# Kernel tuning notes

Hardware: AMD Instinct MI355X
Metric: run time of the kernel (lower is better)

The kernel has to match this reference:

```python
import jax, jax.numpy as jnp
import numpy as np
from jax import lax


def _conv(x, w, padding):
    # NCHW conv, stride 1
    return lax.conv_general_dilated(
        x, w, window_strides=(1, 1), padding=padding,
        dimension_numbers=("NCHW", "OIHW", "NCHW"))


def setup_inputs() -> dict:
    key = jax.random.key(0)
    ks = jax.random.split(key, 6)
    B, C_IN, H, W = 128, 2, 64, 64
    L_H, L_Q = 150, 10
    return {
        "X":   jax.random.normal(ks[0], (B, C_IN, H, W), jnp.float32),
        "h_w": jax.random.normal(ks[1], (L_H, C_IN, 3, 3), jnp.float32) * 0.1,
        "h_b": jax.random.normal(ks[2], (L_H,), jnp.float32) * 0.1,
        "r_w": jax.random.normal(ks[3], (1, L_H, 1, 1), jnp.float32) * 0.1,
        "q_w": jax.random.normal(ks[4], (L_Q, 1, 3, 3), jnp.float32) * 0.1,
        "w":   jax.random.normal(ks[5], (L_Q, 1, 3, 3), jnp.float32) * 0.1,
        "k":   40,
    }


def reference(X, h_w, h_b, r_w, q_w, w, k):
    # h = Conv3x3(X) + bias ; r = Conv1x1(h) ; q = Conv3x3(r)
    h = _conv(X, h_w, "SAME") + h_b[None, :, None, None]   # [B, l_h, H, W]
    r = _conv(h, r_w, "VALID")                             # [B, 1, H, W]
    q = _conv(r, q_w, "SAME")                              # [B, l_q, H, W]
    v = jnp.max(q, axis=1, keepdims=True)                  # [B, 1, H, W]

    qw_cat = jnp.concatenate([q_w, w], axis=1)             # [l_q, 2, 3, 3]

    def body(i, v):
        rv = jnp.concatenate([r, v], axis=1)               # [B, 2, H, W]
        q = _conv(rv, qw_cat, "SAME")                      # [B, l_q, H, W]
        return jnp.max(q, axis=1, keepdims=True)

    v = lax.fori_loop(0, k - 1, body, v)
    return v
```

## Files before the change

### kernel.cpp

```cpp
#include <hip/hip_runtime.h>

typedef float f2 __attribute__((ext_vector_type(2)));

#define HW 64
#define XR (66*64)
#define LH 150
#define LQ 10

__device__ __forceinline__ float dpp_wshr1(float x) {
    return __builtin_bit_cast(float, __builtin_amdgcn_update_dpp(
        0, __builtin_bit_cast(int, x), 0x138, 0xF, 0xF, true));
}
__device__ __forceinline__ float dpp_wshl1(float x) {
    return __builtin_bit_cast(float, __builtin_amdgcn_update_dpp(
        0, __builtin_bit_cast(int, x), 0x130, 0xF, 0xF, true));
}
__device__ __forceinline__ f2 dpp2_shr(f2 v) { return (f2){dpp_wshr1(v.x), dpp_wshr1(v.y)}; }
__device__ __forceinline__ f2 dpp2_shl(f2 v) { return (f2){dpp_wshl1(v.x), dpp_wshl1(v.y)}; }

__device__ __forceinline__ f2 pk_fma_b0(f2 a, f2 wpair, f2 c) {
    f2 d;
    asm("v_pk_fma_f32 %0, %1, %2, %3 op_sel_hi:[1,0,1]"
        : "=v"(d) : "v"(a), "s"(wpair), "v"(c));
    return d;
}
__device__ __forceinline__ f2 pk_fma_b1(f2 a, f2 wpair, f2 c) {
    f2 d;
    asm("v_pk_fma_f32 %0, %1, %2, %3 op_sel:[0,1,0]"
        : "=v"(d) : "v"(a), "s"(wpair), "v"(c));
    return d;
}

__global__ __launch_bounds__(1024)
void vin_main(const float* __restrict__ X,
              const float* __restrict__ h_w,
              const float* __restrict__ h_b,
              const float* __restrict__ r_w,
              const float* __restrict__ q_w,
              const float* __restrict__ wgt,
              const int* __restrict__ kptr,
              float* __restrict__ out) {
    __shared__ float smem[3*XR + 32];
    float* sR  = smem + 2*XR;
    float* sWE = smem + 3*XR;
    float* sHB = smem;
    float* sHT = smem + 2176;

    const int b = blockIdx.x, tid = threadIdx.x;
    const int w = tid >> 6, l = tid & 63;

    for (int i = tid; i < 3*XR + 32; i += 1024) smem[i] = 0.f;
    __syncthreads();

    #pragma unroll
    for (int i = 0; i < 2; ++i) {
        int j = w + 16*i;
        if (j < 19) {
            float s = 0.f;
            #pragma unroll
            for (int u = 0; u < 3; ++u) {
                int t = l + 64*u;
                if (t < LH) {
                    float src = (j < 18) ? h_w[t*18 + j] : h_b[t];
                    s = fmaf(r_w[t], src, s);
                }
            }
            #pragma unroll
            for (int off = 32; off >= 1; off >>= 1)
                s += __shfl_xor(s, off);
            if (l == 0) sWE[j] = s;
        }
    }

    const float* Xb = X + (size_t)b * 2 * HW * HW;
    for (int i = tid; i < 2*64*16; i += 1024) {
        int ch = i >> 10, j = i & 1023, row = j >> 4, c = j & 15;
        float4 v = *(const float4*)(Xb + ((size_t)ch*HW + row)*HW + c*4);
        *(float4*)(smem + ch*XR + (row+1)*64 + c*4) = v;
    }
    __syncthreads();

    float wE[19];
    #pragma unroll
    for (int i = 0; i < 19; ++i) wE[i] = sWE[i];
    float rloc[4];
    {
        float xc[2][6], xl[2][6], xr[2][6];
        #pragma unroll
        for (int ch = 0; ch < 2; ++ch)
            #pragma unroll
            for (int k = 0; k < 6; ++k) {
                xc[ch][k] = smem[ch*XR + (4*w + k)*64 + l];
                xl[ch][k] = dpp_wshr1(xc[ch][k]);
                xr[ch][k] = dpp_wshl1(xc[ch][k]);
            }
        #pragma unroll
        for (int i = 0; i < 4; ++i) {
            float acc = wE[18];
            #pragma unroll
            for (int ch = 0; ch < 2; ++ch)
                #pragma unroll
                for (int dy = 0; dy < 3; ++dy) {
                    acc = fmaf(xl[ch][i+dy], wE[ch*9 + dy*3 + 0], acc);
                    acc = fmaf(xc[ch][i+dy], wE[ch*9 + dy*3 + 1], acc);
                    acc = fmaf(xr[ch][i+dy], wE[ch*9 + dy*3 + 2], acc);
                }
            rloc[i] = acc;
        }
    }
    #pragma unroll
    for (int i = 0; i < 4; ++i) sR[(4*w + i + 1)*64 + l] = rloc[i];
    __syncthreads();

    f2 qr[LQ][2];
    f2 vc[2];
    {
        float rc[6], rl[6], rr2[6];
        #pragma unroll
        for (int k = 0; k < 6; ++k) {
            rc[k]  = sR[(4*w + k)*64 + l];
            rl[k]  = dpp_wshr1(rc[k]);
            rr2[k] = dpp_wshl1(rc[k]);
        }
        float vcur[4];
        #pragma unroll
        for (int a = 0; a < LQ; ++a) {
            float qa[9];
            #pragma unroll
            for (int i = 0; i < 9; ++i) qa[i] = q_w[a*9 + i];
            float acc[4];
            #pragma unroll
            for (int i = 0; i < 4; ++i) {
                float s = 0.f;
                #pragma unroll
                for (int dy = 0; dy < 3; ++dy) {
                    s = fmaf(rl[i+dy],  qa[dy*3 + 0], s);
                    s = fmaf(rc[i+dy],  qa[dy*3 + 1], s);
                    s = fmaf(rr2[i+dy], qa[dy*3 + 2], s);
                }
                acc[i] = s;
                vcur[i] = a ? fmaxf(vcur[i], s) : s;
            }
            qr[a][0] = (f2){acc[0], acc[1]};
            qr[a][1] = (f2){acc[2], acc[3]};
        }
        vc[0] = (f2){vcur[0], vcur[1]};
        vc[1] = (f2){vcur[2], vcur[3]};
    }
    if (tid < 256) {
        int p = tid >> 7, half = (tid >> 6) & 1, ll = tid & 63;
        if (half == 0) sHB[p*1088 + 0*64  + ll] = 0.f;
        else           sHT[p*1088 + 16*64 + ll] = 0.f;
    }

    f2 wv2[LQ][5];
    #pragma unroll
    for (int a = 0; a < LQ; ++a) {
        #pragma unroll
        for (int p = 0; p < 4; ++p)
            wv2[a][p] = (f2){wgt[a*9 + 2*p], wgt[a*9 + 2*p + 1]};
        wv2[a][4] = (f2){wgt[a*9 + 8], 0.f};
    }

    const int km1 = kptr[0] - 1;
    const int wrB = (w+1)*64 + l;
    const int wrT = w*64 + l;
    for (int t = 0; t < km1; ++t) {
        const int p = (t & 1) * 1088;
        sHB[p + wrB] = vc[1].y;
        sHT[p + wrT] = vc[0].x;
        __syncthreads();
        float ht = sHB[p + wrT];
        float hb = sHT[p + wrB];

        f2 P[3];
        P[0] = (f2){ht,       vc[0].x};
        P[1] = (f2){vc[0].y,  vc[1].x};
        P[2] = (f2){vc[1].y,  hb};
        f2 PL[3], PR[3], OL[2], OR[2];
        #pragma unroll
        for (int j = 0; j < 3; ++j) { PL[j] = dpp2_shr(P[j]); PR[j] = dpp2_shl(P[j]); }
        #pragma unroll
        for (int j = 0; j < 2; ++j) { OL[j] = dpp2_shr(vc[j]); OR[j] = dpp2_shl(vc[j]); }

        f2 vn[2];
        #pragma unroll
        for (int a = 0; a < LQ; ++a) {
            #pragma unroll
            for (int j = 0; j < 2; ++j) {
                f2 acc = qr[a][j];
                acc = pk_fma_b0(PL[j],   wv2[a][0], acc);
                acc = pk_fma_b1(P[j],    wv2[a][0], acc);
                acc = pk_fma_b0(PR[j],   wv2[a][1], acc);
                acc = pk_fma_b1(OL[j],   wv2[a][1], acc);
                acc = pk_fma_b0(vc[j],   wv2[a][2], acc);
                acc = pk_fma_b1(OR[j],   wv2[a][2], acc);
                acc = pk_fma_b0(PL[j+1], wv2[a][3], acc);
                acc = pk_fma_b1(P[j+1],  wv2[a][3], acc);
                acc = pk_fma_b0(PR[j+1], wv2[a][4], acc);
                vn[j] = (a == 0) ? acc : __builtin_elementwise_max(vn[j], acc);
            }
        }
        vc[0] = vn[0]; vc[1] = vn[1];
    }

    float* ob = out + (size_t)b*HW*HW + (size_t)(4*w)*HW + l;
    ob[0*HW] = vc[0].x;
    ob[1*HW] = vc[0].y;
    ob[2*HW] = vc[1].x;
    ob[3*HW] = vc[1].y;
}

extern "C" void kernel_launch(void* const* d_in, const int* in_sizes, int n_in,
                              void* d_out, int out_size, void* d_ws, size_t ws_size,
                              hipStream_t stream) {
    const float* X   = (const float*)d_in[0];
    const float* h_w = (const float*)d_in[1];
    const float* h_b = (const float*)d_in[2];
    const float* r_w = (const float*)d_in[3];
    const float* q_w = (const float*)d_in[4];
    const float* w   = (const float*)d_in[5];
    const int*   k   = (const int*)d_in[6];
    float* out = (float*)d_out;

    vin_main<<<128, 1024, 0, stream>>>(X, h_w, h_b, r_w, q_w, w, k, out);
}
```

Baseline: 146.3 us.

## Split each image across two blocks with global-memory halo exchange

Each image is now split into top and bottom halves, one per block, so the launch grows from 128 to 256 blocks and fills more compute units. Each thread now handles 2 rows instead of 4. At every iteration the boundary rows are exchanged between the paired blocks through a global buffer of tagged 64-bit atomics, with spin-waits on the iteration tag. This doubles parallelism at the cost of a per-iteration cross-block global round trip and a memset launch, and it relies on both blocks of a pair being co-resident to avoid deadlock.

After: 123.4 us. 15.7% less time.

```diff
diff --git a/kernel.cpp b/kernel.cpp
--- a/kernel.cpp
+++ b/kernel.cpp
@@ -3,9 +3,14 @@
 typedef float f2 __attribute__((ext_vector_type(2)));
 
 #define HW 64
-#define XR (66*64)
 #define LH 150
 #define LQ 10
+
+#define X36R (36*64)
+#define R34  (34*64)
+#define SMEM_TOT (2*X36R + R34 + 32)
+
+__device__ unsigned long long g_halo[2*2*128*64];
 
 __device__ __forceinline__ float dpp_wshr1(float x) {
     return __builtin_bit_cast(float, __builtin_amdgcn_update_dpp(
@@ -40,16 +45,19 @@
               const float* __restrict__ wgt,
               const int* __restrict__ kptr,
               float* __restrict__ out) {
-    __shared__ float smem[3*XR + 32];
-    float* sR  = smem + 2*XR;
-    float* sWE = smem + 3*XR;
+    __shared__ float smem[SMEM_TOT];
+    float* sR  = smem + 2*X36R;
+    float* sWE = smem + 2*X36R + R34;
     float* sHB = smem;
     float* sHT = smem + 2176;
 
-    const int b = blockIdx.x, tid = threadIdx.x;
+    const int bid = blockIdx.x;
+    const int img = bid & 127, half = bid >> 7;
+    const int base = half << 5;
+    const int tid = threadIdx.x;
     const int w = tid >> 6, l = tid & 63;
 
-    for (int i = tid; i < 3*XR + 32; i += 1024) smem[i] = 0.f;
+    for (int i = tid; i < SMEM_TOT; i += 1024) smem[i] = 0.f;
     __syncthreads();
 
     #pragma unroll
@@ -72,65 +80,59 @@
         }
     }
 
-    const float* Xb = X + (size_t)b * 2 * HW * HW;
-    for (int i = tid; i < 2*64*16; i += 1024) {
-        int ch = i >> 10, j = i & 1023, row = j >> 4, c = j & 15;
-        float4 v = *(const float4*)(Xb + ((size_t)ch*HW + row)*HW + c*4);
-        *(float4*)(smem + ch*XR + (row+1)*64 + c*4) = v;
+    const float* Xb = X + (size_t)img * 2 * HW * HW;
+    const int r0v    = half ? 30 : 0;
+    const int ldsOff = half ? 0  : 2;
+    for (int i = tid; i < 2*34*16; i += 1024) {
+        int ch = i / 544, j = i - ch*544;
+        int row = j >> 4, c = j & 15;
+        float4 v = *(const float4*)(Xb + ((size_t)ch*HW + (r0v + row))*HW + c*4);
+        *(float4*)(smem + ch*X36R + (ldsOff + row)*64 + c*4) = v;
     }
     __syncthreads();
 
     float wE[19];
     #pragma unroll
     for (int i = 0; i < 19; ++i) wE[i] = sWE[i];
-    float rloc[4];
-    {
-        float xc[2][6], xl[2][6], xr[2][6];
-        #pragma unroll
-        for (int ch = 0; ch < 2; ++ch)
-            #pragma unroll
-            for (int k = 0; k < 6; ++k) {
-                xc[ch][k] = smem[ch*XR + (4*w + k)*64 + l];
-                xl[ch][k] = dpp_wshr1(xc[ch][k]);
-                xr[ch][k] = dpp_wshl1(xc[ch][k]);
-            }
-        #pragma unroll
-        for (int i = 0; i < 4; ++i) {
+    for (int j = w; j < 34; j += 16) {
+        int gj = base - 1 + j;
+        if (gj >= 0 && gj < 64) {
             float acc = wE[18];
             #pragma unroll
             for (int ch = 0; ch < 2; ++ch)
                 #pragma unroll
                 for (int dy = 0; dy < 3; ++dy) {
-                    acc = fmaf(xl[ch][i+dy], wE[ch*9 + dy*3 + 0], acc);
-                    acc = fmaf(xc[ch][i+dy], wE[ch*9 + dy*3 + 1], acc);
-                    acc = fmaf(xr[ch][i+dy], wE[ch*9 + dy*3 + 2], acc);
+                    float xc = smem[ch*X36R + (j + dy)*64 + l];
+                    float xl = dpp_wshr1(xc);
+                    float xr = dpp_wshl1(xc);
+                    acc = fmaf(xl, wE[ch*9 + dy*3 + 0], acc);
+                    acc = fmaf(xc, wE[ch*9 + dy*3 + 1], acc);
+                    acc = fmaf(xr, wE[ch*9 + dy*3 + 2], acc);
                 }
-            rloc[i] = acc;
-        }
-    }
-    #pragma unroll
-    for (int i = 0; i < 4; ++i) sR[(4*w + i + 1)*64 + l] = rloc[i];
+            sR[j*64 + l] = acc;
+        }
+    }
     __syncthreads();
 
-    f2 qr[LQ][2];
-    f2 vc[2];
+    f2 qr[LQ];
+    f2 vc;
     {
-        float rc[6], rl[6], rr2[6];
-        #pragma unroll
-        for (int k = 0; k < 6; ++k) {
-            rc[k]  = sR[(4*w + k)*64 + l];
-            rl[k]  = dpp_wshr1(rc[k]);
-            rr2[k] = dpp_wshl1(rc[k]);
-        }
-        float vcur[4];
+        float rc[4], rl[4], rr2[4];
+        #pragma unroll
+        for (int kk = 0; kk < 4; ++kk) {
+            rc[kk]  = sR[(2*w + kk)*64 + l];
+            rl[kk]  = dpp_wshr1(rc[kk]);
+            rr2[kk] = dpp_wshl1(rc[kk]);
+        }
+        float vcur[2];
         #pragma unroll
         for (int a = 0; a < LQ; ++a) {
             float qa[9];
             #pragma unroll
             for (int i = 0; i < 9; ++i) qa[i] = q_w[a*9 + i];
-            float acc[4];
-            #pragma unroll
-            for (int i = 0; i < 4; ++i) {
+            float acc[2];
+            #pragma unroll
+            for (int i = 0; i < 2; ++i) {
                 float s = 0.f;
                 #pragma unroll
                 for (int dy = 0; dy < 3; ++dy) {
@@ -141,16 +143,14 @@
                 acc[i] = s;
                 vcur[i] = a ? fmaxf(vcur[i], s) : s;
             }
-            qr[a][0] = (f2){acc[0], acc[1]};
-            qr[a][1] = (f2){acc[2], acc[3]};
-        }
-        vc[0] = (f2){vcur[0], vcur[1]};
-        vc[1] = (f2){vcur[2], vcur[3]};
+            qr[a] = (f2){acc[0], acc[1]};
+        }
+        vc = (f2){vcur[0], vcur[1]};
     }
     if (tid < 256) {
-        int p = tid >> 7, half = (tid >> 6) & 1, ll = tid & 63;
-        if (half == 0) sHB[p*1088 + 0*64  + ll] = 0.f;
-        else           sHT[p*1088 + 16*64 + ll] = 0.f;
+        int p = tid >> 7, hh = (tid >> 6) & 1, ll = tid & 63;
+        if (hh == 0) sHB[p*1088 + 0*64  + ll] = 0.f;
+        else         sHT[p*1088 + 16*64 + ll] = 0.f;
     }
 
     f2 wv2[LQ][5];
@@ -161,54 +161,81 @@
             wv2[a][p] = (f2){wgt[a*9 + 2*p], wgt[a*9 + 2*p + 1]};
         wv2[a][4] = (f2){wgt[a*9 + 8], 0.f};
     }
+
+    const bool downSend = (half == 0) && (w == 15);
+    const bool upSend   = (half == 1) && (w == 0);
+    unsigned long long* dn = g_halo;
+    unsigned long long* up = g_halo + 2*128*64;
 
     const int km1 = kptr[0] - 1;
     const int wrB = (w+1)*64 + l;
     const int wrT = w*64 + l;
     for (int t = 0; t < km1; ++t) {
-        const int p = (t & 1) * 1088;
-        sHB[p + wrB] = vc[1].y;
-        sHT[p + wrT] = vc[0].x;
-        __syncthreads();
-        float ht = sHB[p + wrT];
-        float hb = sHT[p + wrB];
-
-        f2 P[3];
-        P[0] = (f2){ht,       vc[0].x};
-        P[1] = (f2){vc[0].y,  vc[1].x};
-        P[2] = (f2){vc[1].y,  hb};
-        f2 PL[3], PR[3], OL[2], OR[2];
-        #pragma unroll
-        for (int j = 0; j < 3; ++j) { PL[j] = dpp2_shr(P[j]); PR[j] = dpp2_shl(P[j]); }
-        #pragma unroll
-        for (int j = 0; j < 2; ++j) { OL[j] = dpp2_shr(vc[j]); OR[j] = dpp2_shl(vc[j]); }
-
-        f2 vn[2];
+        const int p = (t & 1);
+        if (downSend) {
+            float vy = vc.y;
+            unsigned long long u = ((unsigned long long)(unsigned)(t + 1) << 32)
+                                 | (unsigned long long)__builtin_bit_cast(unsigned, vy);
+            __hip_atomic_store(&dn[(p*128 + img)*64 + l], u,
+                               __ATOMIC_RELAXED, __HIP_MEMORY_SCOPE_AGENT);
+        }
+        if (upSend) {
+            float vx = vc.x;
+            unsigned long long u = ((unsigned long long)(unsigned)(t + 1) << 32)
+                                 | (unsigned long long)__builtin_bit_cast(unsigned, vx);
+            __hip_atomic_store(&up[(p*128 + img)*64 + l], u,
+                               __ATOMIC_RELAXED, __HIP_MEMORY_SCOPE_AGENT);
+        }
+        sHB[p*1088 + wrB] = vc.y;
+        sHT[p*1088 + wrT] = vc.x;
+        asm volatile("s_waitcnt lgkmcnt(0)" ::: "memory");
+        __builtin_amdgcn_s_barrier();
+        float ht = sHB[p*1088 + wrT];
+        float hb = sHT[p*1088 + wrB];
+        if (upSend) {
+            unsigned long long u;
+            do {
+                u = __hip_atomic_load(&dn[(p*128 + img)*64 + l],
+                                      __ATOMIC_RELAXED, __HIP_MEMORY_SCOPE_AGENT);
+            } while ((unsigned)(u >> 32) != (unsigned)(t + 1));
+            ht = __builtin_bit_cast(float, (unsigned)u);
+        }
+        if (downSend) {
+            unsigned long long u;
+            do {
+                u = __hip_atomic_load(&up[(p*128 + img)*64 + l],
+                                      __ATOMIC_RELAXED, __HIP_MEMORY_SCOPE_AGENT);
+            } while ((unsigned)(u >> 32) != (unsigned)(t + 1));
+            hb = __builtin_bit_cast(float, (unsigned)u);
+        }
+
+        f2 P0 = (f2){ht,   vc.x};
+        f2 P1 = (f2){vc.y, hb};
+        f2 P0L = dpp2_shr(P0), P0R = dpp2_shl(P0);
+        f2 P1L = dpp2_shr(P1), P1R = dpp2_shl(P1);
+        f2 OL  = dpp2_shr(vc), OR_ = dpp2_shl(vc);
+
+        f2 vn;
         #pragma unroll
         for (int a = 0; a < LQ; ++a) {
-            #pragma unroll
-            for (int j = 0; j < 2; ++j) {
-                f2 acc = qr[a][j];
-                acc = pk_fma_b0(PL[j],   wv2[a][0], acc);
-                acc = pk_fma_b1(P[j],    wv2[a][0], acc);
-                acc = pk_fma_b0(PR[j],   wv2[a][1], acc);
-                acc = pk_fma_b1(OL[j],   wv2[a][1], acc);
-                acc = pk_fma_b0(vc[j],   wv2[a][2], acc);
-                acc = pk_fma_b1(OR[j],   wv2[a][2], acc);
-                acc = pk_fma_b0(PL[j+1], wv2[a][3], acc);
-                acc = pk_fma_b1(P[j+1],  wv2[a][3], acc);
-                acc = pk_fma_b0(PR[j+1], wv2[a][4], acc);
-                vn[j] = (a == 0) ? acc : __builtin_elementwise_max(vn[j], acc);
-            }
-        }
-        vc[0] = vn[0]; vc[1] = vn[1];
-    }
-
-    float* ob = out + (size_t)b*HW*HW + (size_t)(4*w)*HW + l;
-    ob[0*HW] = vc[0].x;
-    ob[1*HW] = vc[0].y;
-    ob[2*HW] = vc[1].x;
-    ob[3*HW] = vc[1].y;
+            f2 acc = qr[a];
+            acc = pk_fma_b0(P0L, wv2[a][0], acc);
+            acc = pk_fma_b1(P0,  wv2[a][0], acc);
+            acc = pk_fma_b0(P0R, wv2[a][1], acc);
+            acc = pk_fma_b1(OL,  wv2[a][1], acc);
+            acc = pk_fma_b0(vc,  wv2[a][2], acc);
+            acc = pk_fma_b1(OR_, wv2[a][2], acc);
+            acc = pk_fma_b0(P1L, wv2[a][3], acc);
+            acc = pk_fma_b1(P1,  wv2[a][3], acc);
+            acc = pk_fma_b0(P1R, wv2[a][4], acc);
+            vn = (a == 0) ? acc : __builtin_elementwise_max(vn, acc);
+        }
+        vc = vn;
+    }
+
+    float* ob = out + (size_t)img*HW*HW + (size_t)(base + 2*w)*HW + l;
+    ob[0]  = vc.x;
+    ob[HW] = vc.y;
 }
 
 extern "C" void kernel_launch(void* const* d_in, const int* in_sizes, int n_in,
@@ -222,6 +249,11 @@
     const float* w   = (const float*)d_in[5];
     const int*   k   = (const int*)d_in[6];
     float* out = (float*)d_out;
-
-    vin_main<<<128, 1024, 0, stream>>>(X, h_w, h_b, r_w, q_w, w, k, out);
-}
+    (void)d_ws; (void)ws_size;
+
+    static void* haloPtr = nullptr;
+    if (!haloPtr) hipGetSymbolAddress(&haloPtr, HIP_SYMBOL(g_halo));
+    hipMemsetAsync(haloPtr, 0, sizeof(unsigned long long)*2*2*128*64, stream);
+
+    vin_main<<<256, 1024, 0, stream>>>(X, h_w, h_b, r_w, q_w, w, k, out);
+}
```
